# Kernel optimization log

Measured on AMD Instinct MI355X. Metric: run time of the kernel, lower is better.

Reference implementation:

```python
import jax, jax.numpy as jnp
import numpy as np
import math

SIZE = 64
SCALE = math.sqrt(SIZE)
EPS = 1e-12  # torch F.normalize default eps

def l2_normalize(x, axis):
    n = jnp.linalg.norm(x, ord=2, axis=axis, keepdims=True)
    return x / jnp.maximum(n, EPS)

def setup_inputs() -> dict:
    key = jax.random.key(0)
    k1, k2, k3 = jax.random.split(key, 3)
    n, l, s, d, v = 8, 2048, 2048, SIZE, SIZE
    return {
        "query": jax.random.normal(k1, (n, l, d), dtype=jnp.float32),
        "key": jax.random.normal(k2, (n, s, d), dtype=jnp.float32),
        "value": jax.random.normal(k3, (n, s, v), dtype=jnp.float32),
        "mask": jnp.ones((n, l, s), dtype=bool),
    }

def reference(query, key, value, mask):
    # rank-3 query path with normalize=True (cosine attention)
    q = l2_normalize(query, 2)
    k = l2_normalize(key, 2)
    score = jnp.einsum('nlk,nsk->nls', q, k) / SCALE
    score = jnp.where(mask, score, -jnp.inf)
    score = jax.nn.softmax(score, axis=2)  # [n, l, s]
    # equivalent to (score.unsqueeze(3) * value.unsqueeze(1)).sum(2)
    output_value = jnp.einsum('nls,nsv->nlv', score, value)
    return (output_value, score)
```

## Files before the change

### kernel.cpp

```cpp
#include <hip/hip_runtime.h>
#include <hip/hip_bf16.h>
#include <math.h>


typedef __bf16 bf16x8 __attribute__((ext_vector_type(8)));
typedef __bf16 bf16x4 __attribute__((ext_vector_type(4)));
typedef float f32x4 __attribute__((ext_vector_type(4)));

#define NB 8
#define LL 2048
#define SS 2048
#define DD 64

__global__ __launch_bounds__(256) void prep_norm(const float* __restrict__ q,
                                                 const float* __restrict__ k,
                                                 __bf16* __restrict__ Qb,
                                                 __bf16* __restrict__ Kb) {
  int w = threadIdx.x >> 6, lane = threadIdx.x & 63;
  int r = blockIdx.x * 4 + w;
  const float* src;
  __bf16* dst;
  float extra;
  if (r < NB * LL) {
    src = q + (size_t)r * DD;
    dst = Qb + (size_t)r * DD;
    extra = 0.125f;
  } else {
    int rk = r - NB * LL;
    src = k + (size_t)rk * DD;
    dst = Kb + (size_t)rk * DD;
    extra = 1.0f;
  }
  float x = src[lane];
  float ss = x * x;
  ss += __shfl_xor(ss, 1);
  ss += __shfl_xor(ss, 2);
  ss += __shfl_xor(ss, 4);
  ss += __shfl_xor(ss, 8);
  ss += __shfl_xor(ss, 16);
  ss += __shfl_xor(ss, 32);
  float nrm = sqrtf(ss);
  float sc = extra / fmaxf(nrm, 1e-12f);
  dst[lane] = (__bf16)(x * sc);
}

__global__ __launch_bounds__(256) void prep_vt(const float* __restrict__ v,
                                               __bf16* __restrict__ Vt) {
  __shared__ __bf16 tile[64][72];
  int n = blockIdx.y;
  int s0 = blockIdx.x * 64;
  int t = threadIdx.x;
#pragma unroll
  for (int it = 0; it < 4; ++it) {
    int idx = t + it * 256;
    int s = idx >> 4, c = idx & 15;
    float4 f = *(const float4*)(v + ((size_t)(n * SS + s0 + s)) * DD + c * 4);
    tile[s][c * 4 + 0] = (__bf16)f.x;
    tile[s][c * 4 + 1] = (__bf16)f.y;
    tile[s][c * 4 + 2] = (__bf16)f.z;
    tile[s][c * 4 + 3] = (__bf16)f.w;
  }
  __syncthreads();
#pragma unroll
  for (int it = 0; it < 4; ++it) {
    int idx = t + it * 256;
    int vv = idx >> 4, c = idx & 15;
    bf16x4 o;
    o[0] = tile[c * 4 + 0][vv];
    o[1] = tile[c * 4 + 1][vv];
    o[2] = tile[c * 4 + 2][vv];
    o[3] = tile[c * 4 + 3][vv];
    *(bf16x4*)(Vt + ((size_t)(n * DD + vv)) * SS + s0 + c * 4) = o;
  }
}

__global__ __launch_bounds__(512, 4) void attn_main(const __bf16* __restrict__ Qb,
                                                    const __bf16* __restrict__ Kb,
                                                    const __bf16* __restrict__ Vt,
                                                    const int* __restrict__ mask,
                                                    float* __restrict__ out_val,
                                                    float* __restrict__ out_score) {
  __shared__ __bf16 e_lds[2][16][136];
  __shared__ float rs_lds[8][16];
  __shared__ float acc_red[4][16][17];

  const int n = blockIdx.y;
  const int l0 = blockIdx.x * 16;
  const int t = threadIdx.x;
  const int w = t >> 6;
  const int lane = t & 63;
  const int m16 = lane & 15;
  const int quad = lane >> 4;
  const int vg = w & 3;
  const int sh = (w >> 2) * 64;

  const __bf16* qrow = Qb + ((size_t)(n * LL + l0 + m16)) * DD;
  bf16x8 aq0 = *(const bf16x8*)(qrow + quad * 8);
  bf16x8 aq1 = *(const bf16x8*)(qrow + 32 + quad * 8);

  const __bf16* kbase = Kb + (size_t)n * SS * DD;
  const __bf16* vrow = Vt + ((size_t)(n * DD + vg * 16 + m16)) * SS + sh;
  const size_t mrow = ((size_t)(n * LL + l0 + m16)) * SS + w * 16 + quad * 4;

  f32x4 acc_o = {0.f, 0.f, 0.f, 0.f};
  float rsum = 0.f;
  bf16x4 stash[16];
  int4 mkb[2];
  mkb[0] = *(const int4*)(mask + mrow);
  mkb[1] = *(const int4*)(mask + mrow + 128);

#pragma unroll
  for (int c = 0; c < 16; ++c) {
    const int sc = c * 128;
    const __bf16* krow = kbase + (size_t)(sc + w * 16 + m16) * DD;
    bf16x8 kb0 = *(const bf16x8*)(krow + quad * 8);
    bf16x8 kb1 = *(const bf16x8*)(krow + 32 + quad * 8);
    bf16x8 bv0 = *(const bf16x8*)(vrow + sc + quad * 8);
    bf16x8 bv1 = *(const bf16x8*)(vrow + sc + 32 + quad * 8);
    f32x4 acc = {0.f, 0.f, 0.f, 0.f};
    acc = __builtin_amdgcn_mfma_f32_16x16x32_bf16(kb0, aq0, acc, 0, 0, 0);
    acc = __builtin_amdgcn_mfma_f32_16x16x32_bf16(kb1, aq1, acc, 0, 0, 0);
    const int4 mk = mkb[c & 1];
    if (c + 2 < 16) mkb[c & 1] = *(const int4*)(mask + mrow + (size_t)(c + 2) * 128);
    float e0 = mk.x ? __expf(acc[0]) : 0.f;
    float e1 = mk.y ? __expf(acc[1]) : 0.f;
    float e2 = mk.z ? __expf(acc[2]) : 0.f;
    float e3 = mk.w ? __expf(acc[3]) : 0.f;
    rsum += (e0 + e1) + (e2 + e3);
    bf16x4 sv;
    sv[0] = (__bf16)e0;
    sv[1] = (__bf16)e1;
    sv[2] = (__bf16)e2;
    sv[3] = (__bf16)e3;
    stash[c] = sv;
    *(bf16x4*)(&e_lds[c & 1][m16][w * 16 + quad * 4]) = sv;
    __syncthreads();
    bf16x8 ae0 = *(const bf16x8*)(&e_lds[c & 1][m16][sh + quad * 8]);
    bf16x8 ae1 = *(const bf16x8*)(&e_lds[c & 1][m16][sh + 32 + quad * 8]);
    acc_o = __builtin_amdgcn_mfma_f32_16x16x32_bf16(ae0, bv0, acc_o, 0, 0, 0);
    acc_o = __builtin_amdgcn_mfma_f32_16x16x32_bf16(ae1, bv1, acc_o, 0, 0, 0);
  }

  rsum += __shfl_xor(rsum, 16);
  rsum += __shfl_xor(rsum, 32);
  if (quad == 0) rs_lds[w][m16] = rsum;
  if (w >= 4) {
#pragma unroll
    for (int r = 0; r < 4; ++r) acc_red[vg][quad * 4 + r][m16] = acc_o[r];
  }
  __syncthreads();

  float tot = 0.f;
#pragma unroll
  for (int ww = 0; ww < 8; ++ww) tot += rs_lds[ww][m16];
  const float inv_s = 1.0f / tot;

  if (w < 4) {
#pragma unroll
    for (int r = 0; r < 4; ++r) {
      const int row = quad * 4 + r;
      float tr = 0.f;
#pragma unroll
      for (int ww = 0; ww < 8; ++ww) tr += rs_lds[ww][row];
      const float o = (acc_o[r] + acc_red[vg][row][m16]) / tr;
      out_val[((size_t)(n * LL + l0 + row)) * DD + vg * 16 + m16] = o;
    }
  }

  float* orow = out_score + mrow;
#pragma unroll
  for (int c = 0; c < 16; ++c) {
    float4 o;
    o.x = (float)stash[c][0] * inv_s;
    o.y = (float)stash[c][1] * inv_s;
    o.z = (float)stash[c][2] * inv_s;
    o.w = (float)stash[c][3] * inv_s;
    *(float4*)(orow + (size_t)c * 128) = o;
  }
}

extern "C" void kernel_launch(void* const* d_in, const int* in_sizes, int n_in,
                              void* d_out, int out_size, void* d_ws, size_t ws_size,
                              hipStream_t stream) {
  const float* q = (const float*)d_in[0];
  const float* k = (const float*)d_in[1];
  const float* v = (const float*)d_in[2];
  const int* mask = (const int*)d_in[3];

  float* out_val = (float*)d_out;
  float* out_score = out_val + (size_t)NB * LL * DD;

  __bf16* Qb = (__bf16*)d_ws;
  __bf16* Kb = Qb + (size_t)NB * LL * DD;
  __bf16* Vt = Kb + (size_t)NB * SS * DD;

  prep_norm<<<dim3((NB * LL * 2) / 4), dim3(256), 0, stream>>>(q, k, Qb, Kb);
  prep_vt<<<dim3(SS / 64, NB), dim3(256), 0, stream>>>(v, Vt);
  attn_main<<<dim3(LL / 16, NB), dim3(512), 0, stream>>>(Qb, Kb, Vt, mask, out_val, out_score);
}
```

Measured before the change: 295.4 us.

## Compute PV directly from QK accumulators, drop per-chunk LDS exchange and barriers

The P·V product now uses 16x16x16 bf16 MFMAs that take the QK^T accumulator layout directly as the A operand, so each wave keeps its own full 64-wide output partial. This removes the per-chunk LDS write, __syncthreads and LDS read of the exponentials. The partials of all 8 waves are then summed through a larger LDS buffer at the end. K loads are double-buffered one chunk ahead, and the grid is flattened with a remapped block id so adjacent blocks spread across batches (presumably for XCD/L2 locality). In exchange there are more MFMAs per chunk, more accumulator registers, a bigger final reduction, and an inline asm fallback with a manual s_nop.

```diff
diff --git a/kernel.cpp b/kernel.cpp
--- a/kernel.cpp
+++ b/kernel.cpp
@@ -6,11 +6,25 @@
 typedef __bf16 bf16x8 __attribute__((ext_vector_type(8)));
 typedef __bf16 bf16x4 __attribute__((ext_vector_type(4)));
 typedef float f32x4 __attribute__((ext_vector_type(4)));
+typedef short short4v __attribute__((ext_vector_type(4)));
 
 #define NB 8
 #define LL 2048
 #define SS 2048
 #define DD 64
+
+static __device__ __forceinline__ f32x4 pv_mfma16(bf16x4 a, bf16x4 b, f32x4 c) {
+#if __has_builtin(__builtin_amdgcn_mfma_f32_16x16x16bf16_1k)
+  return __builtin_amdgcn_mfma_f32_16x16x16bf16_1k(
+      __builtin_bit_cast(short4v, a), __builtin_bit_cast(short4v, b), c, 0, 0, 0);
+#else
+  f32x4 d;
+  asm("s_nop 1\n\tv_mfma_f32_16x16x16_bf16 %0, %1, %2, %3"
+      : "=v"(d)
+      : "v"(a), "v"(b), "v"(c));
+  return d;
+#endif
+}
 
 __global__ __launch_bounds__(256) void prep_norm(const float* __restrict__ q,
                                                  const float* __restrict__ k,
@@ -80,43 +94,67 @@
                                                     const int* __restrict__ mask,
                                                     float* __restrict__ out_val,
                                                     float* __restrict__ out_score) {
-  __shared__ __bf16 e_lds[2][16][136];
+  __shared__ float red[8][16][66];
   __shared__ float rs_lds[8][16];
-  __shared__ float acc_red[4][16][17];
-
-  const int n = blockIdx.y;
-  const int l0 = blockIdx.x * 16;
+
+  const int id = blockIdx.x;
+  const int data = (id & 7) * 128 + (id >> 3);
+  const int n = data >> 7;
+  const int l0 = (data & 127) * 16;
+
   const int t = threadIdx.x;
   const int w = t >> 6;
   const int lane = t & 63;
   const int m16 = lane & 15;
   const int quad = lane >> 4;
-  const int vg = w & 3;
-  const int sh = (w >> 2) * 64;
 
   const __bf16* qrow = Qb + ((size_t)(n * LL + l0 + m16)) * DD;
   bf16x8 aq0 = *(const bf16x8*)(qrow + quad * 8);
   bf16x8 aq1 = *(const bf16x8*)(qrow + 32 + quad * 8);
 
   const __bf16* kbase = Kb + (size_t)n * SS * DD;
-  const __bf16* vrow = Vt + ((size_t)(n * DD + vg * 16 + m16)) * SS + sh;
+  const __bf16* vr0 = Vt + ((size_t)(n * DD + 0 * 16 + m16)) * SS + w * 16 + quad * 4;
+  const __bf16* vr1 = Vt + ((size_t)(n * DD + 1 * 16 + m16)) * SS + w * 16 + quad * 4;
+  const __bf16* vr2 = Vt + ((size_t)(n * DD + 2 * 16 + m16)) * SS + w * 16 + quad * 4;
+  const __bf16* vr3 = Vt + ((size_t)(n * DD + 3 * 16 + m16)) * SS + w * 16 + quad * 4;
   const size_t mrow = ((size_t)(n * LL + l0 + m16)) * SS + w * 16 + quad * 4;
 
-  f32x4 acc_o = {0.f, 0.f, 0.f, 0.f};
+  f32x4 acc0 = {0.f, 0.f, 0.f, 0.f};
+  f32x4 acc1 = {0.f, 0.f, 0.f, 0.f};
+  f32x4 acc2 = {0.f, 0.f, 0.f, 0.f};
+  f32x4 acc3 = {0.f, 0.f, 0.f, 0.f};
   float rsum = 0.f;
   bf16x4 stash[16];
   int4 mkb[2];
   mkb[0] = *(const int4*)(mask + mrow);
   mkb[1] = *(const int4*)(mask + mrow + 128);
 
+  bf16x8 k0a, k1a, k0b, k1b;
+  {
+    const __bf16* krow = kbase + (size_t)(w * 16 + m16) * DD;
+    k0a = *(const bf16x8*)(krow + quad * 8);
+    k1a = *(const bf16x8*)(krow + 32 + quad * 8);
+  }
+
 #pragma unroll
   for (int c = 0; c < 16; ++c) {
     const int sc = c * 128;
-    const __bf16* krow = kbase + (size_t)(sc + w * 16 + m16) * DD;
-    bf16x8 kb0 = *(const bf16x8*)(krow + quad * 8);
-    bf16x8 kb1 = *(const bf16x8*)(krow + 32 + quad * 8);
-    bf16x8 bv0 = *(const bf16x8*)(vrow + sc + quad * 8);
-    bf16x8 bv1 = *(const bf16x8*)(vrow + sc + 32 + quad * 8);
+    const bf16x8 kb0 = (c & 1) ? k0b : k0a;
+    const bf16x8 kb1 = (c & 1) ? k1b : k1a;
+    if (c + 1 < 16) {
+      const __bf16* krow = kbase + (size_t)(sc + 128 + w * 16 + m16) * DD;
+      if (c & 1) {
+        k0a = *(const bf16x8*)(krow + quad * 8);
+        k1a = *(const bf16x8*)(krow + 32 + quad * 8);
+      } else {
+        k0b = *(const bf16x8*)(krow + quad * 8);
+        k1b = *(const bf16x8*)(krow + 32 + quad * 8);
+      }
+    }
+    bf16x4 bv0 = *(const bf16x4*)(vr0 + sc);
+    bf16x4 bv1 = *(const bf16x4*)(vr1 + sc);
+    bf16x4 bv2 = *(const bf16x4*)(vr2 + sc);
+    bf16x4 bv3 = *(const bf16x4*)(vr3 + sc);
     f32x4 acc = {0.f, 0.f, 0.f, 0.f};
     acc = __builtin_amdgcn_mfma_f32_16x16x32_bf16(kb0, aq0, acc, 0, 0, 0);
     acc = __builtin_amdgcn_mfma_f32_16x16x32_bf16(kb1, aq1, acc, 0, 0, 0);
@@ -133,39 +171,42 @@
     sv[2] = (__bf16)e2;
     sv[3] = (__bf16)e3;
     stash[c] = sv;
-    *(bf16x4*)(&e_lds[c & 1][m16][w * 16 + quad * 4]) = sv;
-    __syncthreads();
-    bf16x8 ae0 = *(const bf16x8*)(&e_lds[c & 1][m16][sh + quad * 8]);
-    bf16x8 ae1 = *(const bf16x8*)(&e_lds[c & 1][m16][sh + 32 + quad * 8]);
-    acc_o = __builtin_amdgcn_mfma_f32_16x16x32_bf16(ae0, bv0, acc_o, 0, 0, 0);
-    acc_o = __builtin_amdgcn_mfma_f32_16x16x32_bf16(ae1, bv1, acc_o, 0, 0, 0);
+    acc0 = pv_mfma16(sv, bv0, acc0);
+    acc1 = pv_mfma16(sv, bv1, acc1);
+    acc2 = pv_mfma16(sv, bv2, acc2);
+    acc3 = pv_mfma16(sv, bv3, acc3);
   }
 
   rsum += __shfl_xor(rsum, 16);
   rsum += __shfl_xor(rsum, 32);
   if (quad == 0) rs_lds[w][m16] = rsum;
-  if (w >= 4) {
-#pragma unroll
-    for (int r = 0; r < 4; ++r) acc_red[vg][quad * 4 + r][m16] = acc_o[r];
+  asm volatile("s_nop 7");
+#pragma unroll
+  for (int r = 0; r < 4; ++r) {
+    red[w][quad * 4 + r][0 * 16 + m16] = acc0[r];
+    red[w][quad * 4 + r][1 * 16 + m16] = acc1[r];
+    red[w][quad * 4 + r][2 * 16 + m16] = acc2[r];
+    red[w][quad * 4 + r][3 * 16 + m16] = acc3[r];
   }
   __syncthreads();
+
+#pragma unroll
+  for (int i = 0; i < 2; ++i) {
+    const int flat = i * 512 + t;
+    const int l = flat >> 6, vv = flat & 63;
+    float s = 0.f, tr = 0.f;
+#pragma unroll
+    for (int ww = 0; ww < 8; ++ww) {
+      s += red[ww][l][vv];
+      tr += rs_lds[ww][l];
+    }
+    out_val[((size_t)(n * LL + l0 + l)) * DD + vv] = s / tr;
+  }
 
   float tot = 0.f;
 #pragma unroll
   for (int ww = 0; ww < 8; ++ww) tot += rs_lds[ww][m16];
   const float inv_s = 1.0f / tot;
-
-  if (w < 4) {
-#pragma unroll
-    for (int r = 0; r < 4; ++r) {
-      const int row = quad * 4 + r;
-      float tr = 0.f;
-#pragma unroll
-      for (int ww = 0; ww < 8; ++ww) tr += rs_lds[ww][row];
-      const float o = (acc_o[r] + acc_red[vg][row][m16]) / tr;
-      out_val[((size_t)(n * LL + l0 + row)) * DD + vg * 16 + m16] = o;
-    }
-  }
 
   float* orow = out_score + mrow;
 #pragma unroll
@@ -196,5 +237,5 @@
 
   prep_norm<<<dim3((NB * LL * 2) / 4), dim3(256), 0, stream>>>(q, k, Qb, Kb);
   prep_vt<<<dim3(SS / 64, NB), dim3(256), 0, stream>>>(v, Vt);
-  attn_main<<<dim3(LL / 16, NB), dim3(512), 0, stream>>>(Qb, Kb, Vt, mask, out_val, out_score);
-}
+  attn_main<<<dim3((LL / 16) * NB), dim3(512), 0, stream>>>(Qb, Kb, Vt, mask, out_val, out_score);
+}
```

Result: slower. 351.0 us (+18.8%).

## Prefetch K tiles and deeper mask loads, lighter barrier, interleave batches

Applied to the files above, without the earlier changes.

The K tile for the next chunk is now double-buffered in registers, and mask prefetch goes from two chunks ahead to four, to hide global load latency behind the MFMA and exp work. __syncthreads is replaced by an LDS-only waitcnt plus s_barrier, so outstanding global loads no longer have to drain at each step. The grid is flattened so consecutive blocks cycle through batches, which changes how blocks map to batches and may affect cache behavior. The extra prefetched registers raise register pressure, which at the launch bound of 4 blocks could cause spills.

```diff
diff --git a/kernel.cpp b/kernel.cpp
--- a/kernel.cpp
+++ b/kernel.cpp
@@ -84,8 +84,10 @@
   __shared__ float rs_lds[8][16];
   __shared__ float acc_red[4][16][17];
 
-  const int n = blockIdx.y;
-  const int l0 = blockIdx.x * 16;
+  const int id = blockIdx.x;
+  const int n = id & 7;
+  const int l0 = (id >> 3) * 16;
+
   const int t = threadIdx.x;
   const int w = t >> 6;
   const int lane = t & 63;
@@ -101,27 +103,47 @@
   const __bf16* kbase = Kb + (size_t)n * SS * DD;
   const __bf16* vrow = Vt + ((size_t)(n * DD + vg * 16 + m16)) * SS + sh;
   const size_t mrow = ((size_t)(n * LL + l0 + m16)) * SS + w * 16 + quad * 4;
+  const int* mptr = mask + mrow;
 
   f32x4 acc_o = {0.f, 0.f, 0.f, 0.f};
   float rsum = 0.f;
   bf16x4 stash[16];
-  int4 mkb[2];
-  mkb[0] = *(const int4*)(mask + mrow);
-  mkb[1] = *(const int4*)(mask + mrow + 128);
+
+  int4 mkb[4];
+  mkb[0] = *(const int4*)(mptr + 0 * 128);
+  mkb[1] = *(const int4*)(mptr + 1 * 128);
+  mkb[2] = *(const int4*)(mptr + 2 * 128);
+  mkb[3] = *(const int4*)(mptr + 3 * 128);
+
+  bf16x8 kpa0, kpa1, kpb0, kpb1;
+  {
+    const __bf16* kr = kbase + (size_t)(w * 16 + m16) * DD;
+    kpa0 = *(const bf16x8*)(kr + quad * 8);
+    kpa1 = *(const bf16x8*)(kr + 32 + quad * 8);
+  }
 
 #pragma unroll
   for (int c = 0; c < 16; ++c) {
     const int sc = c * 128;
-    const __bf16* krow = kbase + (size_t)(sc + w * 16 + m16) * DD;
-    bf16x8 kb0 = *(const bf16x8*)(krow + quad * 8);
-    bf16x8 kb1 = *(const bf16x8*)(krow + 32 + quad * 8);
+    const bf16x8 kb0 = (c & 1) ? kpb0 : kpa0;
+    const bf16x8 kb1 = (c & 1) ? kpb1 : kpa1;
+    if (c + 1 < 16) {
+      const __bf16* kr = kbase + (size_t)(sc + 128 + w * 16 + m16) * DD;
+      if (c & 1) {
+        kpa0 = *(const bf16x8*)(kr + quad * 8);
+        kpa1 = *(const bf16x8*)(kr + 32 + quad * 8);
+      } else {
+        kpb0 = *(const bf16x8*)(kr + quad * 8);
+        kpb1 = *(const bf16x8*)(kr + 32 + quad * 8);
+      }
+    }
     bf16x8 bv0 = *(const bf16x8*)(vrow + sc + quad * 8);
     bf16x8 bv1 = *(const bf16x8*)(vrow + sc + 32 + quad * 8);
+    const int4 mk = mkb[c & 3];
+    if (c + 4 < 16) mkb[c & 3] = *(const int4*)(mptr + (size_t)(c + 4) * 128);
     f32x4 acc = {0.f, 0.f, 0.f, 0.f};
     acc = __builtin_amdgcn_mfma_f32_16x16x32_bf16(kb0, aq0, acc, 0, 0, 0);
     acc = __builtin_amdgcn_mfma_f32_16x16x32_bf16(kb1, aq1, acc, 0, 0, 0);
-    const int4 mk = mkb[c & 1];
-    if (c + 2 < 16) mkb[c & 1] = *(const int4*)(mask + mrow + (size_t)(c + 2) * 128);
     float e0 = mk.x ? __expf(acc[0]) : 0.f;
     float e1 = mk.y ? __expf(acc[1]) : 0.f;
     float e2 = mk.z ? __expf(acc[2]) : 0.f;
@@ -134,7 +156,8 @@
     sv[3] = (__bf16)e3;
     stash[c] = sv;
     *(bf16x4*)(&e_lds[c & 1][m16][w * 16 + quad * 4]) = sv;
-    __syncthreads();
+    asm volatile("s_waitcnt lgkmcnt(0)" ::: "memory");
+    __builtin_amdgcn_s_barrier();
     bf16x8 ae0 = *(const bf16x8*)(&e_lds[c & 1][m16][sh + quad * 8]);
     bf16x8 ae1 = *(const bf16x8*)(&e_lds[c & 1][m16][sh + 32 + quad * 8]);
     acc_o = __builtin_amdgcn_mfma_f32_16x16x32_bf16(ae0, bv0, acc_o, 0, 0, 0);
@@ -196,5 +219,5 @@
 
   prep_norm<<<dim3((NB * LL * 2) / 4), dim3(256), 0, stream>>>(q, k, Qb, Kb);
   prep_vt<<<dim3(SS / 64, NB), dim3(256), 0, stream>>>(v, Vt);
-  attn_main<<<dim3(LL / 16, NB), dim3(512), 0, stream>>>(Qb, Kb, Vt, mask, out_val, out_score);
-}
+  attn_main<<<dim3((LL / 16) * NB), dim3(512), 0, stream>>>(Qb, Kb, Vt, mask, out_val, out_score);
+}
```

Result: slower. 307.7 us (+4.2%).
